# Optimization experiments

Hardware: AMD Instinct MI355X
Metric: run time of the kernel (lower is better)

## Reference

```python
import jax, jax.numpy as jnp
import numpy as np
import math

H = 48
IN = 8
B = 1048576
DT = 0.1

def setup_inputs() -> dict:
    key = jax.random.key(0)
    ks = jax.random.split(key, 10)
    g = 1.0 / math.sqrt(H)
    hidden = jax.random.normal(ks[0], (B, H), dtype=jnp.float32)
    x = jax.random.normal(ks[1], (IN, B), dtype=jnp.float32)
    P = jax.random.uniform(ks[2], (H, IN), minval=-g, maxval=g, dtype=jnp.float32)
    P_z = jax.random.uniform(ks[3], (H, IN), minval=-g, maxval=g, dtype=jnp.float32)
    K = jax.random.uniform(ks[4], (H, H), minval=0.0, maxval=g, dtype=jnp.float32)
    C = jax.random.uniform(ks[5], (H, H), minval=0.0, maxval=g, dtype=jnp.float32)
    b_v = jnp.zeros((H, 1), dtype=jnp.float32)
    b_z = jnp.full((H, 1), math.log(1.0 / 99.0), dtype=jnp.float32)
    e_e = jax.random.uniform(ks[6], (1,), dtype=jnp.float32)
    e_i = -jax.random.uniform(ks[7], (1,), dtype=jnp.float32)
    return {"hidden": hidden, "x": x, "P": P, "b_v": b_v, "K": K, "C": C,
            "P_z": P_z, "b_z": b_z, "e_e": e_e, "e_i": e_i}

def _input_mask():
    # rows [H/4, H/2) and [3H/4, H) receive no input
    rows = jnp.arange(H)
    keep = ~(((rows >= H // 4) & (rows < H // 2)) | (rows >= 3 * H // 4))
    return keep.astype(jnp.float32)[:, None]  # (H, 1)

def reference(hidden, x, P, b_v, K, C, P_z, b_z, e_e, e_i):
    # hidden: (B, H) -> v: (H, B)
    v = hidden.T
    r = jax.nn.sigmoid(v)                      # (H, B)
    Ksp = jax.nn.softplus(K)                   # (H, H)
    Csp = jax.nn.softplus(C)
    S = Ksp + Csp
    W_E = jax.nn.relu(e_e * S[:, : H // 2])    # excitatory columns >= 0
    W_I = -jax.nn.relu(-(e_i * S[:, H // 2 :]))  # inhibitory columns <= 0
    W = jnp.concatenate((W_E, W_I), axis=1)    # (H, H)
    P_masked = P * _input_mask()               # (H, IN)
    z = DT * jax.nn.sigmoid(Ksp @ r + P_z @ x + b_z)           # (H, B)
    v_new = (1.0 - z) * v + DT * (W @ r + P_masked @ x + b_v)  # (H, B)
    return v_new.T                             # (B, H)
```

## Files before the change

kernel.cpp:

```cpp
#include <hip/hip_runtime.h>
#include <math.h>


#define DTC 0.1f

typedef __attribute__((ext_vector_type(8))) short bf16x8;
typedef __attribute__((ext_vector_type(4))) float f32x4;

__device__ __forceinline__ unsigned bf16_rn(float f) {
    unsigned u = __float_as_uint(f);
    u += 0x7FFFu + ((u >> 16) & 1u);
    return u >> 16;
}

__device__ __forceinline__ float fast_sigmoid(float v) {
    const float e = __expf(-v);
    return __builtin_amdgcn_rcpf(1.0f + e);
}

__global__ void prep_kernel(const float* __restrict__ P,
                            const float* __restrict__ b_v,
                            const float* __restrict__ K,
                            const float* __restrict__ C,
                            const float* __restrict__ P_z,
                            const float* __restrict__ b_z,
                            const float* __restrict__ e_e,
                            const float* __restrict__ e_i,
                            unsigned short* __restrict__ ws16)
{
    const float ee = e_e[0];
    const float ei = e_i[0];
    for (int idx = threadIdx.x; idx < 6144; idx += blockDim.x) {
        const int fi  = idx >> 9;
        const int rem = idx & 511;
        const int l   = rem >> 3;
        const int j   = rem & 7;
        const int mt  = fi >> 1;
        const int ks  = fi & 1;
        const int m   = mt * 16 + (l & 15);
        const int k   = ks * 32 + ((l >> 4) << 3) + j;
        const bool zp = (m < 48);
        const int h   = zp ? m : m - 48;
        float val;
        if (k < 48) {
            const float ksp = log1pf(expf(K[h * 48 + k]));
            if (zp) {
                val = ksp;
            } else {
                const float S = ksp + log1pf(expf(C[h * 48 + k]));
                val = (k < 24) ? fmaxf(0.0f, ee * S) : fminf(0.0f, ei * S);
            }
        } else if (k < 56) {
            const int jj = k - 48;
            if (zp) {
                val = P_z[h * 8 + jj];
            } else {
                const float mask = ((h / 12) & 1) ? 0.0f : 1.0f;
                val = P[h * 8 + jj] * mask;
            }
        } else if (k == 56) {
            val = zp ? b_z[h] : b_v[h];
        } else {
            val = 0.0f;
        }
        ws16[idx] = (unsigned short)bf16_rn(val);
    }
}

__global__ void __launch_bounds__(256)
dale_main(const float* __restrict__ hidden,
          const float* __restrict__ x,
          const unsigned short* __restrict__ ws16,
          float* __restrict__ out,
          int B)
{
    __shared__ unsigned lds[256 * 32];
    const int tid  = threadIdx.x;
    const int wave = tid >> 6;
    const int lane = tid & 63;
    const long bb  = (long)blockIdx.x * 256;

    {
        const long gb = (bb + tid < (long)B) ? (bb + tid) : (long)B - 1;
        const float4* hp = reinterpret_cast<const float4*>(hidden + gb * 48);
        const unsigned rowbase = tid * 32;
        const unsigned sw = (tid & 7);
        #pragma unroll
        for (int c = 0; c < 6; ++c) {
            const float4 a = hp[2 * c];
            const float4 b = hp[2 * c + 1];
            uint4 w;
            w.x = bf16_rn(fast_sigmoid(a.x)) | (bf16_rn(fast_sigmoid(a.y)) << 16);
            w.y = bf16_rn(fast_sigmoid(a.z)) | (bf16_rn(fast_sigmoid(a.w)) << 16);
            w.z = bf16_rn(fast_sigmoid(b.x)) | (bf16_rn(fast_sigmoid(b.y)) << 16);
            w.w = bf16_rn(fast_sigmoid(b.z)) | (bf16_rn(fast_sigmoid(b.w)) << 16);
            *reinterpret_cast<uint4*>(&lds[rowbase + 4 * (c ^ sw)]) = w;
        }
        {
            float xv[8];
            #pragma unroll
            for (int j = 0; j < 8; ++j) xv[j] = x[(long)j * B + gb];
            uint4 w6;
            w6.x = bf16_rn(xv[0]) | (bf16_rn(xv[1]) << 16);
            w6.y = bf16_rn(xv[2]) | (bf16_rn(xv[3]) << 16);
            w6.z = bf16_rn(xv[4]) | (bf16_rn(xv[5]) << 16);
            w6.w = bf16_rn(xv[6]) | (bf16_rn(xv[7]) << 16);
            *reinterpret_cast<uint4*>(&lds[rowbase + 4 * (6 ^ sw)]) = w6;
            uint4 w7;
            w7.x = 0x00003F80u;
            w7.y = 0u; w7.z = 0u; w7.w = 0u;
            *reinterpret_cast<uint4*>(&lds[rowbase + 4 * (7 ^ sw)]) = w7;
        }
    }
    __syncthreads();

    bf16x8 A[12];
    {
        const bf16x8* ap = reinterpret_cast<const bf16x8*>(ws16);
        #pragma unroll
        for (int i = 0; i < 12; ++i) A[i] = ap[i * 64 + lane];
    }

    #pragma unroll 1
    for (int s = 0; s < 4; ++s) {
        const int row = wave * 64 + s * 16 + (lane & 15);
        const unsigned rsw = (row & 7);
        const unsigned c0 = (unsigned)(lane >> 4);
        const bf16x8 B0 = *reinterpret_cast<const bf16x8*>(&lds[row * 32 + 4 * (c0 ^ rsw)]);
        const bf16x8 B1 = *reinterpret_cast<const bf16x8*>(&lds[row * 32 + 4 * ((c0 + 4) ^ rsw)]);

        f32x4 acc[6];
        #pragma unroll
        for (int t = 0; t < 6; ++t) acc[t] = (f32x4){0.f, 0.f, 0.f, 0.f};
        #pragma unroll
        for (int t = 0; t < 6; ++t) {
            acc[t] = __builtin_amdgcn_mfma_f32_16x16x32_bf16(A[t * 2 + 0], B0, acc[t], 0, 0, 0);
            acc[t] = __builtin_amdgcn_mfma_f32_16x16x32_bf16(A[t * 2 + 1], B1, acc[t], 0, 0, 0);
        }

        const long ge = bb + row;
        const bool ok = (ge < (long)B);
        const long gc = ok ? ge : (long)B - 1;
        const float4* vp = reinterpret_cast<const float4*>(hidden + gc * 48) + (lane >> 4);
        float4*       op = reinterpret_cast<float4*>(out + gc * 48) + (lane >> 4);
        #pragma unroll
        for (int t = 0; t < 3; ++t) {
            const float4 v = vp[t * 4];
            const f32x4 az = acc[t];
            const f32x4 av = acc[t + 3];
            float4 o;
            o.x = fmaf(DTC, av[0], v.x * (1.0f - DTC * fast_sigmoid(az[0])));
            o.y = fmaf(DTC, av[1], v.y * (1.0f - DTC * fast_sigmoid(az[1])));
            o.z = fmaf(DTC, av[2], v.z * (1.0f - DTC * fast_sigmoid(az[2])));
            o.w = fmaf(DTC, av[3], v.w * (1.0f - DTC * fast_sigmoid(az[3])));
            if (ok) op[t * 4] = o;
        }
    }
}

extern "C" void kernel_launch(void* const* d_in, const int* in_sizes, int n_in,
                              void* d_out, int out_size, void* d_ws, size_t ws_size,
                              hipStream_t stream) {
    const float* hidden = (const float*)d_in[0];
    const float* x      = (const float*)d_in[1];
    const float* P      = (const float*)d_in[2];
    const float* b_v    = (const float*)d_in[3];
    const float* K      = (const float*)d_in[4];
    const float* C      = (const float*)d_in[5];
    const float* P_z    = (const float*)d_in[6];
    const float* b_z    = (const float*)d_in[7];
    const float* e_e    = (const float*)d_in[8];
    const float* e_i    = (const float*)d_in[9];
    float* out = (float*)d_out;
    unsigned short* ws16 = (unsigned short*)d_ws;
    const int B = in_sizes[0] / 48;

    prep_kernel<<<dim3(1), dim3(256), 0, stream>>>(P, b_v, K, C, P_z, b_z, e_e, e_i, ws16);
    dale_main<<<dim3((B + 255) / 256), dim3(256), 0, stream>>>(hidden, x, ws16, out, B);
}
```

Baseline: 418.3 us.

## Make waves persistent over tiles with register prefetch and LDS-cached hidden

Each wave now loops over 8 tiles of 32 batch rows and prefetches the next tile's hidden and x into registers while computing the current one. The block-wide syncthreads is replaced by per-wave LDS buffers. Hidden values are also kept in LDS so the epilogue no longer re-reads them from global memory. The change drops bounds checks and assumes B is divisible by 1024, and it raises register pressure under a launch bound of 3 blocks per SM.

Measured after the change: 396.4 us. 1.06x faster.

```diff
diff --git a/kernel.cpp b/kernel.cpp
--- a/kernel.cpp
+++ b/kernel.cpp
@@ -3,6 +3,7 @@
 
 
 #define DTC 0.1f
+#define TPW 8
 
 typedef __attribute__((ext_vector_type(8))) short bf16x8;
 typedef __attribute__((ext_vector_type(4))) float f32x4;
@@ -16,6 +17,15 @@
 __device__ __forceinline__ float fast_sigmoid(float v) {
     const float e = __expf(-v);
     return __builtin_amdgcn_rcpf(1.0f + e);
+}
+
+__device__ __forceinline__ uint4 pack_sig(const float4 a, const float4 b) {
+    uint4 w;
+    w.x = bf16_rn(fast_sigmoid(a.x)) | (bf16_rn(fast_sigmoid(a.y)) << 16);
+    w.y = bf16_rn(fast_sigmoid(a.z)) | (bf16_rn(fast_sigmoid(a.w)) << 16);
+    w.z = bf16_rn(fast_sigmoid(b.x)) | (bf16_rn(fast_sigmoid(b.y)) << 16);
+    w.w = bf16_rn(fast_sigmoid(b.z)) | (bf16_rn(fast_sigmoid(b.w)) << 16);
+    return w;
 }
 
 __global__ void prep_kernel(const float* __restrict__ P,
@@ -67,52 +77,22 @@
     }
 }
 
-__global__ void __launch_bounds__(256)
+__global__ void __launch_bounds__(256, 3)
 dale_main(const float* __restrict__ hidden,
           const float* __restrict__ x,
           const unsigned short* __restrict__ ws16,
           float* __restrict__ out,
           int B)
 {
-    __shared__ unsigned lds[256 * 32];
+    __shared__ unsigned r_lds[4][32 * 32];
+    __shared__ float    v_lds[4][32 * 52];
     const int tid  = threadIdx.x;
     const int wave = tid >> 6;
     const int lane = tid & 63;
-    const long bb  = (long)blockIdx.x * 256;
-
-    {
-        const long gb = (bb + tid < (long)B) ? (bb + tid) : (long)B - 1;
-        const float4* hp = reinterpret_cast<const float4*>(hidden + gb * 48);
-        const unsigned rowbase = tid * 32;
-        const unsigned sw = (tid & 7);
-        #pragma unroll
-        for (int c = 0; c < 6; ++c) {
-            const float4 a = hp[2 * c];
-            const float4 b = hp[2 * c + 1];
-            uint4 w;
-            w.x = bf16_rn(fast_sigmoid(a.x)) | (bf16_rn(fast_sigmoid(a.y)) << 16);
-            w.y = bf16_rn(fast_sigmoid(a.z)) | (bf16_rn(fast_sigmoid(a.w)) << 16);
-            w.z = bf16_rn(fast_sigmoid(b.x)) | (bf16_rn(fast_sigmoid(b.y)) << 16);
-            w.w = bf16_rn(fast_sigmoid(b.z)) | (bf16_rn(fast_sigmoid(b.w)) << 16);
-            *reinterpret_cast<uint4*>(&lds[rowbase + 4 * (c ^ sw)]) = w;
-        }
-        {
-            float xv[8];
-            #pragma unroll
-            for (int j = 0; j < 8; ++j) xv[j] = x[(long)j * B + gb];
-            uint4 w6;
-            w6.x = bf16_rn(xv[0]) | (bf16_rn(xv[1]) << 16);
-            w6.y = bf16_rn(xv[2]) | (bf16_rn(xv[3]) << 16);
-            w6.z = bf16_rn(xv[4]) | (bf16_rn(xv[5]) << 16);
-            w6.w = bf16_rn(xv[6]) | (bf16_rn(xv[7]) << 16);
-            *reinterpret_cast<uint4*>(&lds[rowbase + 4 * (6 ^ sw)]) = w6;
-            uint4 w7;
-            w7.x = 0x00003F80u;
-            w7.y = 0u; w7.z = 0u; w7.w = 0u;
-            *reinterpret_cast<uint4*>(&lds[rowbase + 4 * (7 ^ sw)]) = w7;
-        }
-    }
-    __syncthreads();
+    const int el   = lane >> 1;
+    const int p    = lane & 1;
+    unsigned* rl = r_lds[wave];
+    float*    vl = v_lds[wave];
 
     bf16x8 A[12];
     {
@@ -121,39 +101,94 @@
         for (int i = 0; i < 12; ++i) A[i] = ap[i * 64 + lane];
     }
 
+    const long wt0 = ((long)blockIdx.x * 4 + wave) * TPW;
+
+    float4 H[6]; float X[8];
+    {
+        const long eb = wt0 * 32;
+        const float4* hp = reinterpret_cast<const float4*>(hidden + (eb + el) * 48) + p * 6;
+        #pragma unroll
+        for (int i = 0; i < 6; ++i) H[i] = hp[i];
+        if (p) {
+            #pragma unroll
+            for (int j = 0; j < 8; ++j) X[j] = x[(long)j * B + eb + el];
+        }
+    }
+
     #pragma unroll 1
-    for (int s = 0; s < 4; ++s) {
-        const int row = wave * 64 + s * 16 + (lane & 15);
-        const unsigned rsw = (row & 7);
-        const unsigned c0 = (unsigned)(lane >> 4);
-        const bf16x8 B0 = *reinterpret_cast<const bf16x8*>(&lds[row * 32 + 4 * (c0 ^ rsw)]);
-        const bf16x8 B1 = *reinterpret_cast<const bf16x8*>(&lds[row * 32 + 4 * ((c0 + 4) ^ rsw)]);
-
-        f32x4 acc[6];
+    for (int it = 0; it < TPW; ++it) {
+        const long eb = (wt0 + it) * 32;
+
+        const unsigned rowbase = el * 32;
+        const unsigned sw = el & 7;
         #pragma unroll
-        for (int t = 0; t < 6; ++t) acc[t] = (f32x4){0.f, 0.f, 0.f, 0.f};
-        #pragma unroll
-        for (int t = 0; t < 6; ++t) {
-            acc[t] = __builtin_amdgcn_mfma_f32_16x16x32_bf16(A[t * 2 + 0], B0, acc[t], 0, 0, 0);
-            acc[t] = __builtin_amdgcn_mfma_f32_16x16x32_bf16(A[t * 2 + 1], B1, acc[t], 0, 0, 0);
-        }
-
-        const long ge = bb + row;
-        const bool ok = (ge < (long)B);
-        const long gc = ok ? ge : (long)B - 1;
-        const float4* vp = reinterpret_cast<const float4*>(hidden + gc * 48) + (lane >> 4);
-        float4*       op = reinterpret_cast<float4*>(out + gc * 48) + (lane >> 4);
-        #pragma unroll
-        for (int t = 0; t < 3; ++t) {
-            const float4 v = vp[t * 4];
-            const f32x4 az = acc[t];
-            const f32x4 av = acc[t + 3];
-            float4 o;
-            o.x = fmaf(DTC, av[0], v.x * (1.0f - DTC * fast_sigmoid(az[0])));
-            o.y = fmaf(DTC, av[1], v.y * (1.0f - DTC * fast_sigmoid(az[1])));
-            o.z = fmaf(DTC, av[2], v.z * (1.0f - DTC * fast_sigmoid(az[2])));
-            o.w = fmaf(DTC, av[3], v.w * (1.0f - DTC * fast_sigmoid(az[3])));
-            if (ok) op[t * 4] = o;
+        for (int c = 0; c < 3; ++c) {
+            const uint4 w = pack_sig(H[2 * c], H[2 * c + 1]);
+            *reinterpret_cast<uint4*>(&rl[rowbase + 4 * (((p * 3 + c)) ^ sw)]) = w;
+        }
+        if (p) {
+            uint4 w6;
+            w6.x = bf16_rn(X[0]) | (bf16_rn(X[1]) << 16);
+            w6.y = bf16_rn(X[2]) | (bf16_rn(X[3]) << 16);
+            w6.z = bf16_rn(X[4]) | (bf16_rn(X[5]) << 16);
+            w6.w = bf16_rn(X[6]) | (bf16_rn(X[7]) << 16);
+            *reinterpret_cast<uint4*>(&rl[rowbase + 4 * (6 ^ sw)]) = w6;
+        } else {
+            uint4 w7;
+            w7.x = 0x00003F80u; w7.y = 0u; w7.z = 0u; w7.w = 0u;
+            *reinterpret_cast<uint4*>(&rl[rowbase + 4 * (7 ^ sw)]) = w7;
+        }
+        {
+            float* vrow = vl + el * 52 + p * 24;
+            #pragma unroll
+            for (int i = 0; i < 6; ++i)
+                *reinterpret_cast<float4*>(vrow + 4 * i) = H[i];
+        }
+
+        if (it + 1 < TPW) {
+            const long nb = (wt0 + it + 1) * 32;
+            const float4* hp = reinterpret_cast<const float4*>(hidden + (nb + el) * 48) + p * 6;
+            #pragma unroll
+            for (int i = 0; i < 6; ++i) H[i] = hp[i];
+            if (p) {
+                #pragma unroll
+                for (int j = 0; j < 8; ++j) X[j] = x[(long)j * B + nb + el];
+            }
+        }
+        __builtin_amdgcn_sched_barrier(0);
+
+        #pragma unroll 1
+        for (int s = 0; s < 2; ++s) {
+            const int row = s * 16 + (lane & 15);
+            const unsigned rsw = row & 7;
+            const unsigned c0 = (unsigned)(lane >> 4);
+            const bf16x8 B0 = *reinterpret_cast<const bf16x8*>(&rl[row * 32 + 4 * (c0 ^ rsw)]);
+            const bf16x8 B1 = *reinterpret_cast<const bf16x8*>(&rl[row * 32 + 4 * ((c0 + 4) ^ rsw)]);
+
+            f32x4 acc[6];
+            #pragma unroll
+            for (int t = 0; t < 6; ++t) acc[t] = (f32x4){0.f, 0.f, 0.f, 0.f};
+            #pragma unroll
+            for (int t = 0; t < 6; ++t) {
+                acc[t] = __builtin_amdgcn_mfma_f32_16x16x32_bf16(A[t * 2 + 0], B0, acc[t], 0, 0, 0);
+                acc[t] = __builtin_amdgcn_mfma_f32_16x16x32_bf16(A[t * 2 + 1], B1, acc[t], 0, 0, 0);
+            }
+
+            const long ge = eb + row;
+            const float* vp = vl + row * 52 + (lane >> 4) * 4;
+            float4* op = reinterpret_cast<float4*>(out + ge * 48) + (lane >> 4);
+            #pragma unroll
+            for (int t = 0; t < 3; ++t) {
+                const float4 v = *reinterpret_cast<const float4*>(vp + 16 * t);
+                const f32x4 az = acc[t];
+                const f32x4 av = acc[t + 3];
+                float4 o;
+                o.x = fmaf(DTC, av[0], v.x * (1.0f - DTC * fast_sigmoid(az[0])));
+                o.y = fmaf(DTC, av[1], v.y * (1.0f - DTC * fast_sigmoid(az[1])));
+                o.z = fmaf(DTC, av[2], v.z * (1.0f - DTC * fast_sigmoid(az[2])));
+                o.w = fmaf(DTC, av[3], v.w * (1.0f - DTC * fast_sigmoid(az[3])));
+                op[t * 4] = o;
+            }
         }
     }
 }
@@ -176,5 +211,6 @@
     const int B = in_sizes[0] / 48;
 
     prep_kernel<<<dim3(1), dim3(256), 0, stream>>>(P, b_v, K, C, P_z, b_z, e_e, e_i, ws16);
-    dale_main<<<dim3((B + 255) / 256), dim3(256), 0, stream>>>(hidden, x, ws16, out, B);
-}
+    const int nblocks = B / (4 * TPW * 32);
+    dale_main<<<dim3(nblocks), dim3(256), 0, stream>>>(hidden, x, ws16, out, B);
+}
```
